# Performance work log

Hardware: AMD Instinct MI355X
Metric: run time of the kernel (lower is better)

Reference implementation:

```python
import jax, jax.numpy as jnp
import numpy as np

B, T, D, H = 256, 1024, 128, 128

def setup_inputs() -> dict:
    key = jax.random.key(0)
    k1, k2, k3, k4 = jax.random.split(key, 4)
    return {
        "x": jax.random.normal(k1, (B, T, D), dtype=jnp.float32),
        "w": jax.random.normal(k2, (D, H), dtype=jnp.float32) * 0.05,
        "state_weight": jax.random.normal(k3, (H, H), dtype=jnp.float32) * 0.05,
        "b": jax.random.normal(k4, (H,), dtype=jnp.float32) * 0.05,
    }

def reference(x, w, state_weight, b):
    # Faithful Elman RNN with return_sequences=False.
    # Original transposes input to time-major [T, B, D], initializes the
    # state from step 0 WITHOUT a recurrent term, then iterates steps 1..T-1.
    X = jnp.transpose(x, (1, 0, 2))  # [T, B, D]
    # Precompute input projections for all steps in one big GEMM (same math).
    proj = jnp.einsum("tbd,dh->tbh", X, w) + b  # [T, B, H]
    state0 = jnp.tanh(proj[0])

    def step(state, pt):
        y = jnp.tanh(pt + state @ state_weight)
        return y, None

    final_state, _ = jax.lax.scan(step, state0, proj[1:])
    return final_state  # [B, H]
```

## Files before the change

kernel.cpp:

```cpp
#include <hip/hip_runtime.h>

#define T_N 1024
#define H_N 128
#define CH   64
#define NCH (T_N / CH)
#define WPAD 136
#define PPAD 68

typedef __attribute__((ext_vector_type(8))) short bf16x8;
typedef __attribute__((ext_vector_type(4))) float f32x4;

__device__ __forceinline__ short f2bf_rne(float f) {
    union { float f; unsigned int i; } v; v.f = f;
    unsigned int r = v.i + 0x7FFFu + ((v.i >> 16) & 1u);
    return (short)(r >> 16);
}
__device__ __forceinline__ float tanh_fast(float x) {
    return 1.0f - 2.0f / (__expf(2.0f * x) + 1.0f);
}

__global__ __launch_bounds__(256, 1) void k_fused(const float* __restrict__ x,
                                                  const float* __restrict__ w,
                                                  const float* __restrict__ wst,
                                                  const float* __restrict__ bias,
                                                  float* __restrict__ out) {
    __shared__ __align__(16) short wT[H_N * WPAD];
    __shared__ __align__(16) float pT[H_N * PPAD];
    __shared__ __align__(16) short sst[2][H_N];

    const int tid  = threadIdx.x;
    const int wv   = tid >> 6;
    const int lane = tid & 63;
    const int l = lane & 15;
    const int q = lane >> 4;
    const int r = blockIdx.x;
    const float* xrow = x + (size_t)r * T_N * H_N;
    const f32x4 zero4 = (f32x4){0.f, 0.f, 0.f, 0.f};

    const float* xlane = xrow + (size_t)(wv * 16 + l) * H_N + q * 8;
    float4 xst[8];
    #pragma unroll
    for (int ks = 0; ks < 4; ++ks) {
        xst[ks * 2 + 0] = *reinterpret_cast<const float4*>(xlane + ks * 32);
        xst[ks * 2 + 1] = *reinterpret_cast<const float4*>(xlane + ks * 32 + 4);
    }

    short* wsT = reinterpret_cast<short*>(pT);
    for (int e = tid * 4; e < H_N * H_N; e += 1024) {
        int k = e >> 7, n = e & 127;
        float4 a4 = *reinterpret_cast<const float4*>(wst + e);
        wsT[(n + 0) * WPAD + k] = f2bf_rne(a4.x);
        wsT[(n + 1) * WPAD + k] = f2bf_rne(a4.y);
        wsT[(n + 2) * WPAD + k] = f2bf_rne(a4.z);
        wsT[(n + 3) * WPAD + k] = f2bf_rne(a4.w);
    }
    __syncthreads();

    bf16x8 wf[2][4];
    #pragma unroll
    for (int b = 0; b < 2; ++b)
        #pragma unroll
        for (int ks = 0; ks < 4; ++ks)
            wf[b][ks] = *reinterpret_cast<const bf16x8*>(
                &wsT[(16 * (2 * wv + b) + l) * WPAD + ks * 32 + q * 8]);
    __syncthreads();

    for (int e = tid * 4; e < H_N * H_N; e += 1024) {
        int k = e >> 7, n = e & 127;
        float4 a4 = *reinterpret_cast<const float4*>(w + e);
        wT[(n + 0) * WPAD + k] = f2bf_rne(a4.x);
        wT[(n + 1) * WPAD + k] = f2bf_rne(a4.y);
        wT[(n + 2) * WPAD + k] = f2bf_rne(a4.z);
        wT[(n + 3) * WPAD + k] = f2bf_rne(a4.w);
    }

    float bv[8];
    #pragma unroll
    for (int nt = 0; nt < 8; ++nt) bv[nt] = bias[nt * 16 + l];

    int par = 0;
    float y0 = 0.f, y1 = 0.f;
    const int row0 = (32 * wv + l) * PPAD;
    const int row1 = (32 * wv + 16 + l) * PPAD;

    #pragma unroll 1
    for (int c = 0; c < NCH; ++c) {
        bf16x8 ax[4];
        #pragma unroll
        for (int ks = 0; ks < 4; ++ks) {
            float4 u0 = xst[ks * 2 + 0];
            float4 u1 = xst[ks * 2 + 1];
            bf16x8 f;
            f[0] = f2bf_rne(u0.x); f[1] = f2bf_rne(u0.y);
            f[2] = f2bf_rne(u0.z); f[3] = f2bf_rne(u0.w);
            f[4] = f2bf_rne(u1.x); f[5] = f2bf_rne(u1.y);
            f[6] = f2bf_rne(u1.z); f[7] = f2bf_rne(u1.w);
            ax[ks] = f;
        }

        if (c + 1 < NCH) {
            const float* pn = xlane + (size_t)(c + 1) * CH * H_N;
            #pragma unroll
            for (int ks = 0; ks < 4; ++ks) {
                xst[ks * 2 + 0] = *reinterpret_cast<const float4*>(pn + ks * 32);
                xst[ks * 2 + 1] = *reinterpret_cast<const float4*>(pn + ks * 32 + 4);
            }
        }

        __syncthreads();

        #pragma unroll
        for (int nt = 0; nt < 8; ++nt) {
            f32x4 acc;
            #pragma unroll
            for (int ks = 0; ks < 4; ++ks) {
                bf16x8 bw = *reinterpret_cast<const bf16x8*>(
                    &wT[(nt * 16 + l) * WPAD + ks * 32 + q * 8]);
                acc = __builtin_amdgcn_mfma_f32_16x16x32_bf16(
                    ax[ks], bw, ks == 0 ? zero4 : acc, 0, 0, 0);
            }
            f32x4 o = (f32x4){acc[0] + bv[nt], acc[1] + bv[nt],
                              acc[2] + bv[nt], acc[3] + bv[nt]};
            *reinterpret_cast<f32x4*>(&pT[(nt * 16 + l) * PPAD + wv * 16 + q * 4]) = o;
        }

        __syncthreads();

        int tstart = 0;
        if (c == 0) {
            if (tid < 128)
                sst[0][tid] = f2bf_rne(tanh_fast(pT[tid * PPAD + 0]));
            __syncthreads();
            tstart = 1;
            par = 0;
        }

        float p0 = pT[row0 + tstart];
        float p1 = pT[row1 + tstart];

        #pragma unroll 1
        for (int t = tstart; t < CH; ++t) {
            bf16x8 a[4];
            #pragma unroll
            for (int ks = 0; ks < 4; ++ks)
                a[ks] = *reinterpret_cast<const bf16x8*>(&sst[par][ks * 32 + q * 8]);

            f32x4 acc[8];
            #pragma unroll
            for (int ks = 0; ks < 4; ++ks) {
                acc[ks]     = __builtin_amdgcn_mfma_f32_16x16x32_bf16(a[ks], wf[0][ks], zero4, 0, 0, 0);
                acc[4 + ks] = __builtin_amdgcn_mfma_f32_16x16x32_bf16(a[ks], wf[1][ks], zero4, 0, 0, 0);
            }

            int tn = (t + 1 < CH) ? t + 1 : t;
            float np0 = pT[row0 + tn];
            float np1 = pT[row1 + tn];

            float z0 = p0 + ((acc[0][0] + acc[1][0]) + (acc[2][0] + acc[3][0]));
            float z1 = p1 + ((acc[4][0] + acc[5][0]) + (acc[6][0] + acc[7][0]));
            y0 = tanh_fast(z0);
            y1 = tanh_fast(z1);
            sst[par ^ 1][32 * wv + l]      = f2bf_rne(y0);
            sst[par ^ 1][32 * wv + 16 + l] = f2bf_rne(y1);
            p0 = np0; p1 = np1;
            par ^= 1;
            __syncthreads();
        }
    }

    if (q == 0) {
        out[r * H_N + 32 * wv + l]      = y0;
        out[r * H_N + 32 * wv + 16 + l] = y1;
    }
}

extern "C" void kernel_launch(void* const* d_in, const int* in_sizes, int n_in,
                              void* d_out, int out_size, void* d_ws, size_t ws_size,
                              hipStream_t stream) {
    const float* x    = (const float*)d_in[0];
    const float* w    = (const float*)d_in[1];
    const float* wst  = (const float*)d_in[2];
    const float* bias = (const float*)d_in[3];
    float* out = (float*)d_out;

    k_fused<<<256, 256, 0, stream>>>(x, w, wst, bias, out);
}
```

Before: 444.4 us.

## Specialize waves: one runs the barrier-free recurrence, one projects the next chunk

The block shrinks to two wavefronts. Wave 0 holds the whole recurrent weight matrix in registers and runs every recurrence step alone. Because only one wave touches the state, the per-step __syncthreads and the double-buffered state disappear. Wave 1 computes the input projection for the next 64-step chunk into a double-buffered LDS tile, so that work overlaps the recurrence. In exchange, each step issues 32 serial MFMAs from a single wave instead of 8 per wave across four waves, which may lengthen the dependent chain per step.

```diff
diff --git a/kernel.cpp b/kernel.cpp
--- a/kernel.cpp
+++ b/kernel.cpp
@@ -5,7 +5,7 @@
 #define CH   64
 #define NCH (T_N / CH)
 #define WPAD 136
-#define PPAD 68
+#define TPAD 68
 
 typedef __attribute__((ext_vector_type(8))) short bf16x8;
 typedef __attribute__((ext_vector_type(4))) float f32x4;
@@ -19,14 +19,14 @@
     return 1.0f - 2.0f / (__expf(2.0f * x) + 1.0f);
 }
 
-__global__ __launch_bounds__(256, 1) void k_fused(const float* __restrict__ x,
+__global__ __launch_bounds__(128, 1) void k_fused(const float* __restrict__ x,
                                                   const float* __restrict__ w,
                                                   const float* __restrict__ wst,
                                                   const float* __restrict__ bias,
                                                   float* __restrict__ out) {
     __shared__ __align__(16) short wT[H_N * WPAD];
-    __shared__ __align__(16) float pT[H_N * PPAD];
-    __shared__ __align__(16) short sst[2][H_N];
+    __shared__ __align__(16) float pT[2][H_N * TPAD];
+    __shared__ __align__(16) short sst[H_N];
 
     const int tid  = threadIdx.x;
     const int wv   = tid >> 6;
@@ -37,35 +37,16 @@
     const float* xrow = x + (size_t)r * T_N * H_N;
     const f32x4 zero4 = (f32x4){0.f, 0.f, 0.f, 0.f};
 
-    const float* xlane = xrow + (size_t)(wv * 16 + l) * H_N + q * 8;
-    float4 xst[8];
-    #pragma unroll
-    for (int ks = 0; ks < 4; ++ks) {
-        xst[ks * 2 + 0] = *reinterpret_cast<const float4*>(xlane + ks * 32);
-        xst[ks * 2 + 1] = *reinterpret_cast<const float4*>(xlane + ks * 32 + 4);
-    }
-
-    short* wsT = reinterpret_cast<short*>(pT);
-    for (int e = tid * 4; e < H_N * H_N; e += 1024) {
+    short* wsTs = reinterpret_cast<short*>(&pT[0][0]);
+    for (int e = tid * 4; e < H_N * H_N; e += 512) {
         int k = e >> 7, n = e & 127;
         float4 a4 = *reinterpret_cast<const float4*>(wst + e);
-        wsT[(n + 0) * WPAD + k] = f2bf_rne(a4.x);
-        wsT[(n + 1) * WPAD + k] = f2bf_rne(a4.y);
-        wsT[(n + 2) * WPAD + k] = f2bf_rne(a4.z);
-        wsT[(n + 3) * WPAD + k] = f2bf_rne(a4.w);
+        wsTs[(n + 0) * WPAD + k] = f2bf_rne(a4.x);
+        wsTs[(n + 1) * WPAD + k] = f2bf_rne(a4.y);
+        wsTs[(n + 2) * WPAD + k] = f2bf_rne(a4.z);
+        wsTs[(n + 3) * WPAD + k] = f2bf_rne(a4.w);
     }
-    __syncthreads();
-
-    bf16x8 wf[2][4];
-    #pragma unroll
-    for (int b = 0; b < 2; ++b)
-        #pragma unroll
-        for (int ks = 0; ks < 4; ++ks)
-            wf[b][ks] = *reinterpret_cast<const bf16x8*>(
-                &wsT[(16 * (2 * wv + b) + l) * WPAD + ks * 32 + q * 8]);
-    __syncthreads();
-
-    for (int e = tid * 4; e < H_N * H_N; e += 1024) {
+    for (int e = tid * 4; e < H_N * H_N; e += 512) {
         int k = e >> 7, n = e & 127;
         float4 a4 = *reinterpret_cast<const float4*>(w + e);
         wT[(n + 0) * WPAD + k] = f2bf_rne(a4.x);
@@ -78,99 +59,116 @@
     #pragma unroll
     for (int nt = 0; nt < 8; ++nt) bv[nt] = bias[nt * 16 + l];
 
-    int par = 0;
+    __syncthreads();
+
+    auto do_chunk = [&](int cc, float* buf) {
+        const float* xc = xrow + (size_t)cc * CH * H_N + (size_t)l * H_N + q * 8;
+        #pragma unroll 1
+        for (int tile = 0; tile < 4; ++tile) {
+            const float* xp = xc + (size_t)tile * 16 * H_N;
+            float4 u[8];
+            #pragma unroll
+            for (int ks = 0; ks < 4; ++ks) {
+                u[2 * ks]     = *reinterpret_cast<const float4*>(xp + ks * 32);
+                u[2 * ks + 1] = *reinterpret_cast<const float4*>(xp + ks * 32 + 4);
+            }
+            bf16x8 ax[4];
+            #pragma unroll
+            for (int ks = 0; ks < 4; ++ks) {
+                float4 u0 = u[2 * ks], u1 = u[2 * ks + 1];
+                bf16x8 f;
+                f[0] = f2bf_rne(u0.x); f[1] = f2bf_rne(u0.y);
+                f[2] = f2bf_rne(u0.z); f[3] = f2bf_rne(u0.w);
+                f[4] = f2bf_rne(u1.x); f[5] = f2bf_rne(u1.y);
+                f[6] = f2bf_rne(u1.z); f[7] = f2bf_rne(u1.w);
+                ax[ks] = f;
+            }
+            #pragma unroll
+            for (int nt = 0; nt < 8; ++nt) {
+                f32x4 acc;
+                #pragma unroll
+                for (int ks = 0; ks < 4; ++ks) {
+                    bf16x8 bw = *reinterpret_cast<const bf16x8*>(
+                        &wT[(nt * 16 + l) * WPAD + ks * 32 + q * 8]);
+                    acc = __builtin_amdgcn_mfma_f32_16x16x32_bf16(
+                        ax[ks], bw, ks == 0 ? zero4 : acc, 0, 0, 0);
+                }
+                f32x4 o = (f32x4){acc[0] + bv[nt], acc[1] + bv[nt],
+                                  acc[2] + bv[nt], acc[3] + bv[nt]};
+                *reinterpret_cast<f32x4*>(
+                    &buf[(nt * 16 + l) * TPAD + tile * 16 + 4 * q]) = o;
+            }
+        }
+    };
+
+    bf16x8 wf[8][4];
+    if (wv == 0) {
+        #pragma unroll
+        for (int nt = 0; nt < 8; ++nt)
+            #pragma unroll
+            for (int ks = 0; ks < 4; ++ks)
+                wf[nt][ks] = *reinterpret_cast<const bf16x8*>(
+                    &wsTs[(16 * nt + l) * WPAD + ks * 32 + q * 8]);
+    } else {
+        do_chunk(0, &pT[1][0]);
+    }
+    __syncthreads();
+
     float y0 = 0.f, y1 = 0.f;
-    const int row0 = (32 * wv + l) * PPAD;
-    const int row1 = (32 * wv + 16 + l) * PPAD;
+    const int row0 = (32 * q + l) * TPAD;
+    const int row1 = (32 * q + 16 + l) * TPAD;
 
     #pragma unroll 1
     for (int c = 0; c < NCH; ++c) {
-        bf16x8 ax[4];
-        #pragma unroll
-        for (int ks = 0; ks < 4; ++ks) {
-            float4 u0 = xst[ks * 2 + 0];
-            float4 u1 = xst[ks * 2 + 1];
-            bf16x8 f;
-            f[0] = f2bf_rne(u0.x); f[1] = f2bf_rne(u0.y);
-            f[2] = f2bf_rne(u0.z); f[3] = f2bf_rne(u0.w);
-            f[4] = f2bf_rne(u1.x); f[5] = f2bf_rne(u1.y);
-            f[6] = f2bf_rne(u1.z); f[7] = f2bf_rne(u1.w);
-            ax[ks] = f;
+        if (wv == 0) {
+            float* pc = &pT[(c + 1) & 1][0];
+            int ts = 0;
+            if (c == 0) {
+                sst[lane]      = f2bf_rne(tanh_fast(pc[lane * TPAD]));
+                sst[64 + lane] = f2bf_rne(tanh_fast(pc[(64 + lane) * TPAD]));
+                ts = 1;
+            }
+            float p0 = pc[row0 + ts];
+            float p1 = pc[row1 + ts];
+            #pragma unroll 1
+            for (int t = ts; t < CH; ++t) {
+                bf16x8 a[4];
+                #pragma unroll
+                for (int ks = 0; ks < 4; ++ks)
+                    a[ks] = *reinterpret_cast<const bf16x8*>(&sst[ks * 32 + q * 8]);
+
+                f32x4 acc[8];
+                #pragma unroll
+                for (int nt = 0; nt < 8; ++nt) {
+                    #pragma unroll
+                    for (int ks = 0; ks < 4; ++ks)
+                        acc[nt] = __builtin_amdgcn_mfma_f32_16x16x32_bf16(
+                            a[ks], wf[nt][ks], ks == 0 ? zero4 : acc[nt], 0, 0, 0);
+                }
+
+                int tn = (t + 1 < CH) ? t + 1 : t;
+                float np0 = pc[row0 + tn];
+                float np1 = pc[row1 + tn];
+
+                float v0 = (q == 0) ? acc[0][0] : (q == 1) ? acc[2][0]
+                         : (q == 2) ? acc[4][0] : acc[6][0];
+                float v1 = (q == 0) ? acc[1][0] : (q == 1) ? acc[3][0]
+                         : (q == 2) ? acc[5][0] : acc[7][0];
+                y0 = tanh_fast(p0 + v0);
+                y1 = tanh_fast(p1 + v1);
+                sst[32 * q + l]      = f2bf_rne(y0);
+                sst[32 * q + 16 + l] = f2bf_rne(y1);
+                p0 = np0; p1 = np1;
+            }
+        } else if (c + 1 < NCH) {
+            do_chunk(c + 1, &pT[c & 1][0]);
         }
-
-        if (c + 1 < NCH) {
-            const float* pn = xlane + (size_t)(c + 1) * CH * H_N;
-            #pragma unroll
-            for (int ks = 0; ks < 4; ++ks) {
-                xst[ks * 2 + 0] = *reinterpret_cast<const float4*>(pn + ks * 32);
-                xst[ks * 2 + 1] = *reinterpret_cast<const float4*>(pn + ks * 32 + 4);
-            }
-        }
-
         __syncthreads();
-
-        #pragma unroll
-        for (int nt = 0; nt < 8; ++nt) {
-            f32x4 acc;
-            #pragma unroll
-            for (int ks = 0; ks < 4; ++ks) {
-                bf16x8 bw = *reinterpret_cast<const bf16x8*>(
-                    &wT[(nt * 16 + l) * WPAD + ks * 32 + q * 8]);
-                acc = __builtin_amdgcn_mfma_f32_16x16x32_bf16(
-                    ax[ks], bw, ks == 0 ? zero4 : acc, 0, 0, 0);
-            }
-            f32x4 o = (f32x4){acc[0] + bv[nt], acc[1] + bv[nt],
-                              acc[2] + bv[nt], acc[3] + bv[nt]};
-            *reinterpret_cast<f32x4*>(&pT[(nt * 16 + l) * PPAD + wv * 16 + q * 4]) = o;
-        }
-
-        __syncthreads();
-
-        int tstart = 0;
-        if (c == 0) {
-            if (tid < 128)
-                sst[0][tid] = f2bf_rne(tanh_fast(pT[tid * PPAD + 0]));
-            __syncthreads();
-            tstart = 1;
-            par = 0;
-        }
-
-        float p0 = pT[row0 + tstart];
-        float p1 = pT[row1 + tstart];
-
-        #pragma unroll 1
-        for (int t = tstart; t < CH; ++t) {
-            bf16x8 a[4];
-            #pragma unroll
-            for (int ks = 0; ks < 4; ++ks)
-                a[ks] = *reinterpret_cast<const bf16x8*>(&sst[par][ks * 32 + q * 8]);
-
-            f32x4 acc[8];
-            #pragma unroll
-            for (int ks = 0; ks < 4; ++ks) {
-                acc[ks]     = __builtin_amdgcn_mfma_f32_16x16x32_bf16(a[ks], wf[0][ks], zero4, 0, 0, 0);
-                acc[4 + ks] = __builtin_amdgcn_mfma_f32_16x16x32_bf16(a[ks], wf[1][ks], zero4, 0, 0, 0);
-            }
-
-            int tn = (t + 1 < CH) ? t + 1 : t;
-            float np0 = pT[row0 + tn];
-            float np1 = pT[row1 + tn];
-
-            float z0 = p0 + ((acc[0][0] + acc[1][0]) + (acc[2][0] + acc[3][0]));
-            float z1 = p1 + ((acc[4][0] + acc[5][0]) + (acc[6][0] + acc[7][0]));
-            y0 = tanh_fast(z0);
-            y1 = tanh_fast(z1);
-            sst[par ^ 1][32 * wv + l]      = f2bf_rne(y0);
-            sst[par ^ 1][32 * wv + 16 + l] = f2bf_rne(y1);
-            p0 = np0; p1 = np1;
-            par ^= 1;
-            __syncthreads();
-        }
     }
 
-    if (q == 0) {
-        out[r * H_N + 32 * wv + l]      = y0;
-        out[r * H_N + 32 * wv + 16 + l] = y1;
+    if (wv == 0) {
+        out[r * H_N + 32 * q + l]      = y0;
+        out[r * H_N + 32 * q + 16 + l] = y1;
     }
 }
 
@@ -183,5 +181,5 @@
     const float* bias = (const float*)d_in[3];
     float* out = (float*)d_out;
 
-    k_fused<<<256, 256, 0, stream>>>(x, w, wst, bias, out);
+    k_fused<<<256, 128, 0, stream>>>(x, w, wst, bias, out);
 }
```

After: 642.0 us. 1.44x slower.

## Process two batch rows per block to interleave independent recurrences

Applied to the files above, without the earlier changes.

Each block now handles two batch rows, running their recurrent MFMA chains side by side inside the same time-step loop, and the grid is halved to 128 blocks. The goal is to hide MFMA and LDS latency in the serial per-step chain by giving each wave independent work, and to share one barrier per step across two sequences. The cost is more registers and LDS (a second projection buffer and state buffer), and only 128 of the device's CUs are used where there were 256 before, so throughput can drop if per-step latency is not the bottleneck.

```diff
diff --git a/kernel.cpp b/kernel.cpp
--- a/kernel.cpp
+++ b/kernel.cpp
@@ -25,34 +25,41 @@
                                                   const float* __restrict__ bias,
                                                   float* __restrict__ out) {
     __shared__ __align__(16) short wT[H_N * WPAD];
-    __shared__ __align__(16) float pT[H_N * PPAD];
-    __shared__ __align__(16) short sst[2][H_N];
+    __shared__ __align__(16) float pTA[H_N * PPAD];
+    __shared__ __align__(16) float pTB[H_N * PPAD];
+    __shared__ __align__(16) short sstA[2][H_N];
+    __shared__ __align__(16) short sstB[2][H_N];
 
     const int tid  = threadIdx.x;
     const int wv   = tid >> 6;
     const int lane = tid & 63;
     const int l = lane & 15;
     const int q = lane >> 4;
-    const int r = blockIdx.x;
-    const float* xrow = x + (size_t)r * T_N * H_N;
+    const int r0 = blockIdx.x * 2;
+    const int r1 = r0 + 1;
+    const float* xrowA = x + (size_t)r0 * T_N * H_N;
+    const float* xrowB = x + (size_t)r1 * T_N * H_N;
     const f32x4 zero4 = (f32x4){0.f, 0.f, 0.f, 0.f};
 
-    const float* xlane = xrow + (size_t)(wv * 16 + l) * H_N + q * 8;
-    float4 xst[8];
+    const float* xlaneA = xrowA + (size_t)(wv * 16 + l) * H_N + q * 8;
+    const float* xlaneB = xrowB + (size_t)(wv * 16 + l) * H_N + q * 8;
+    float4 xstA[8], xstB[8];
     #pragma unroll
     for (int ks = 0; ks < 4; ++ks) {
-        xst[ks * 2 + 0] = *reinterpret_cast<const float4*>(xlane + ks * 32);
-        xst[ks * 2 + 1] = *reinterpret_cast<const float4*>(xlane + ks * 32 + 4);
-    }
-
-    short* wsT = reinterpret_cast<short*>(pT);
+        xstA[ks * 2 + 0] = *reinterpret_cast<const float4*>(xlaneA + ks * 32);
+        xstA[ks * 2 + 1] = *reinterpret_cast<const float4*>(xlaneA + ks * 32 + 4);
+        xstB[ks * 2 + 0] = *reinterpret_cast<const float4*>(xlaneB + ks * 32);
+        xstB[ks * 2 + 1] = *reinterpret_cast<const float4*>(xlaneB + ks * 32 + 4);
+    }
+
+    short* wsTs = reinterpret_cast<short*>(pTA);
     for (int e = tid * 4; e < H_N * H_N; e += 1024) {
         int k = e >> 7, n = e & 127;
         float4 a4 = *reinterpret_cast<const float4*>(wst + e);
-        wsT[(n + 0) * WPAD + k] = f2bf_rne(a4.x);
-        wsT[(n + 1) * WPAD + k] = f2bf_rne(a4.y);
-        wsT[(n + 2) * WPAD + k] = f2bf_rne(a4.z);
-        wsT[(n + 3) * WPAD + k] = f2bf_rne(a4.w);
+        wsTs[(n + 0) * WPAD + k] = f2bf_rne(a4.x);
+        wsTs[(n + 1) * WPAD + k] = f2bf_rne(a4.y);
+        wsTs[(n + 2) * WPAD + k] = f2bf_rne(a4.z);
+        wsTs[(n + 3) * WPAD + k] = f2bf_rne(a4.w);
     }
     __syncthreads();
 
@@ -62,7 +69,7 @@
         #pragma unroll
         for (int ks = 0; ks < 4; ++ks)
             wf[b][ks] = *reinterpret_cast<const bf16x8*>(
-                &wsT[(16 * (2 * wv + b) + l) * WPAD + ks * 32 + q * 8]);
+                &wsTs[(16 * (2 * wv + b) + l) * WPAD + ks * 32 + q * 8]);
     __syncthreads();
 
     for (int e = tid * 4; e < H_N * H_N; e += 1024) {
@@ -79,31 +86,40 @@
     for (int nt = 0; nt < 8; ++nt) bv[nt] = bias[nt * 16 + l];
 
     int par = 0;
-    float y0 = 0.f, y1 = 0.f;
+    float yA0 = 0.f, yA1 = 0.f, yB0 = 0.f, yB1 = 0.f;
     const int row0 = (32 * wv + l) * PPAD;
     const int row1 = (32 * wv + 16 + l) * PPAD;
 
     #pragma unroll 1
     for (int c = 0; c < NCH; ++c) {
-        bf16x8 ax[4];
+        bf16x8 axA[4], axB[4];
         #pragma unroll
         for (int ks = 0; ks < 4; ++ks) {
-            float4 u0 = xst[ks * 2 + 0];
-            float4 u1 = xst[ks * 2 + 1];
+            float4 u0 = xstA[ks * 2 + 0], u1 = xstA[ks * 2 + 1];
             bf16x8 f;
             f[0] = f2bf_rne(u0.x); f[1] = f2bf_rne(u0.y);
             f[2] = f2bf_rne(u0.z); f[3] = f2bf_rne(u0.w);
             f[4] = f2bf_rne(u1.x); f[5] = f2bf_rne(u1.y);
             f[6] = f2bf_rne(u1.z); f[7] = f2bf_rne(u1.w);
-            ax[ks] = f;
+            axA[ks] = f;
+            float4 v0 = xstB[ks * 2 + 0], v1 = xstB[ks * 2 + 1];
+            bf16x8 g;
+            g[0] = f2bf_rne(v0.x); g[1] = f2bf_rne(v0.y);
+            g[2] = f2bf_rne(v0.z); g[3] = f2bf_rne(v0.w);
+            g[4] = f2bf_rne(v1.x); g[5] = f2bf_rne(v1.y);
+            g[6] = f2bf_rne(v1.z); g[7] = f2bf_rne(v1.w);
+            axB[ks] = g;
         }
 
         if (c + 1 < NCH) {
-            const float* pn = xlane + (size_t)(c + 1) * CH * H_N;
-            #pragma unroll
-            for (int ks = 0; ks < 4; ++ks) {
-                xst[ks * 2 + 0] = *reinterpret_cast<const float4*>(pn + ks * 32);
-                xst[ks * 2 + 1] = *reinterpret_cast<const float4*>(pn + ks * 32 + 4);
+            const float* pnA = xlaneA + (size_t)(c + 1) * CH * H_N;
+            const float* pnB = xlaneB + (size_t)(c + 1) * CH * H_N;
+            #pragma unroll
+            for (int ks = 0; ks < 4; ++ks) {
+                xstA[ks * 2 + 0] = *reinterpret_cast<const float4*>(pnA + ks * 32);
+                xstA[ks * 2 + 1] = *reinterpret_cast<const float4*>(pnA + ks * 32 + 4);
+                xstB[ks * 2 + 0] = *reinterpret_cast<const float4*>(pnB + ks * 32);
+                xstB[ks * 2 + 1] = *reinterpret_cast<const float4*>(pnB + ks * 32 + 4);
             }
         }
 
@@ -111,17 +127,22 @@
 
         #pragma unroll
         for (int nt = 0; nt < 8; ++nt) {
-            f32x4 acc;
+            f32x4 aA, aB;
             #pragma unroll
             for (int ks = 0; ks < 4; ++ks) {
                 bf16x8 bw = *reinterpret_cast<const bf16x8*>(
                     &wT[(nt * 16 + l) * WPAD + ks * 32 + q * 8]);
-                acc = __builtin_amdgcn_mfma_f32_16x16x32_bf16(
-                    ax[ks], bw, ks == 0 ? zero4 : acc, 0, 0, 0);
-            }
-            f32x4 o = (f32x4){acc[0] + bv[nt], acc[1] + bv[nt],
-                              acc[2] + bv[nt], acc[3] + bv[nt]};
-            *reinterpret_cast<f32x4*>(&pT[(nt * 16 + l) * PPAD + wv * 16 + q * 4]) = o;
+                aA = __builtin_amdgcn_mfma_f32_16x16x32_bf16(
+                    axA[ks], bw, ks == 0 ? zero4 : aA, 0, 0, 0);
+                aB = __builtin_amdgcn_mfma_f32_16x16x32_bf16(
+                    axB[ks], bw, ks == 0 ? zero4 : aB, 0, 0, 0);
+            }
+            f32x4 oA = (f32x4){aA[0] + bv[nt], aA[1] + bv[nt],
+                               aA[2] + bv[nt], aA[3] + bv[nt]};
+            f32x4 oB = (f32x4){aB[0] + bv[nt], aB[1] + bv[nt],
+                               aB[2] + bv[nt], aB[3] + bv[nt]};
+            *reinterpret_cast<f32x4*>(&pTA[(nt * 16 + l) * PPAD + wv * 16 + q * 4]) = oA;
+            *reinterpret_cast<f32x4*>(&pTB[(nt * 16 + l) * PPAD + wv * 16 + q * 4]) = oB;
         }
 
         __syncthreads();
@@ -129,48 +150,75 @@
         int tstart = 0;
         if (c == 0) {
             if (tid < 128)
-                sst[0][tid] = f2bf_rne(tanh_fast(pT[tid * PPAD + 0]));
+                sstA[0][tid] = f2bf_rne(tanh_fast(pTA[tid * PPAD + 0]));
+            else {
+                int u = tid - 128;
+                sstB[0][u] = f2bf_rne(tanh_fast(pTB[u * PPAD + 0]));
+            }
             __syncthreads();
             tstart = 1;
             par = 0;
         }
 
-        float p0 = pT[row0 + tstart];
-        float p1 = pT[row1 + tstart];
+        float pA0 = pTA[row0 + tstart];
+        float pA1 = pTA[row1 + tstart];
+        float pB0 = pTB[row0 + tstart];
+        float pB1 = pTB[row1 + tstart];
 
         #pragma unroll 1
         for (int t = tstart; t < CH; ++t) {
-            bf16x8 a[4];
+            bf16x8 aA[4], aB[4];
             #pragma unroll
             for (int ks = 0; ks < 4; ++ks)
-                a[ks] = *reinterpret_cast<const bf16x8*>(&sst[par][ks * 32 + q * 8]);
-
-            f32x4 acc[8];
-            #pragma unroll
-            for (int ks = 0; ks < 4; ++ks) {
-                acc[ks]     = __builtin_amdgcn_mfma_f32_16x16x32_bf16(a[ks], wf[0][ks], zero4, 0, 0, 0);
-                acc[4 + ks] = __builtin_amdgcn_mfma_f32_16x16x32_bf16(a[ks], wf[1][ks], zero4, 0, 0, 0);
+                aA[ks] = *reinterpret_cast<const bf16x8*>(&sstA[par][ks * 32 + q * 8]);
+            #pragma unroll
+            for (int ks = 0; ks < 4; ++ks)
+                aB[ks] = *reinterpret_cast<const bf16x8*>(&sstB[par][ks * 32 + q * 8]);
+
+            f32x4 accA[8];
+            #pragma unroll
+            for (int ks = 0; ks < 4; ++ks) {
+                accA[ks]     = __builtin_amdgcn_mfma_f32_16x16x32_bf16(aA[ks], wf[0][ks], zero4, 0, 0, 0);
+                accA[4 + ks] = __builtin_amdgcn_mfma_f32_16x16x32_bf16(aA[ks], wf[1][ks], zero4, 0, 0, 0);
+            }
+            f32x4 accB[8];
+            #pragma unroll
+            for (int ks = 0; ks < 4; ++ks) {
+                accB[ks]     = __builtin_amdgcn_mfma_f32_16x16x32_bf16(aB[ks], wf[0][ks], zero4, 0, 0, 0);
+                accB[4 + ks] = __builtin_amdgcn_mfma_f32_16x16x32_bf16(aB[ks], wf[1][ks], zero4, 0, 0, 0);
             }
 
             int tn = (t + 1 < CH) ? t + 1 : t;
-            float np0 = pT[row0 + tn];
-            float np1 = pT[row1 + tn];
-
-            float z0 = p0 + ((acc[0][0] + acc[1][0]) + (acc[2][0] + acc[3][0]));
-            float z1 = p1 + ((acc[4][0] + acc[5][0]) + (acc[6][0] + acc[7][0]));
-            y0 = tanh_fast(z0);
-            y1 = tanh_fast(z1);
-            sst[par ^ 1][32 * wv + l]      = f2bf_rne(y0);
-            sst[par ^ 1][32 * wv + 16 + l] = f2bf_rne(y1);
-            p0 = np0; p1 = np1;
+            float npA0 = pTA[row0 + tn];
+            float npA1 = pTA[row1 + tn];
+            float npB0 = pTB[row0 + tn];
+            float npB1 = pTB[row1 + tn];
+
+            float zA0 = pA0 + ((accA[0][0] + accA[1][0]) + (accA[2][0] + accA[3][0]));
+            float zA1 = pA1 + ((accA[4][0] + accA[5][0]) + (accA[6][0] + accA[7][0]));
+            yA0 = tanh_fast(zA0);
+            yA1 = tanh_fast(zA1);
+            sstA[par ^ 1][32 * wv + l]      = f2bf_rne(yA0);
+            sstA[par ^ 1][32 * wv + 16 + l] = f2bf_rne(yA1);
+
+            float zB0 = pB0 + ((accB[0][0] + accB[1][0]) + (accB[2][0] + accB[3][0]));
+            float zB1 = pB1 + ((accB[4][0] + accB[5][0]) + (accB[6][0] + accB[7][0]));
+            yB0 = tanh_fast(zB0);
+            yB1 = tanh_fast(zB1);
+            sstB[par ^ 1][32 * wv + l]      = f2bf_rne(yB0);
+            sstB[par ^ 1][32 * wv + 16 + l] = f2bf_rne(yB1);
+
+            pA0 = npA0; pA1 = npA1; pB0 = npB0; pB1 = npB1;
             par ^= 1;
             __syncthreads();
         }
     }
 
     if (q == 0) {
-        out[r * H_N + 32 * wv + l]      = y0;
-        out[r * H_N + 32 * wv + 16 + l] = y1;
+        out[r0 * H_N + 32 * wv + l]      = yA0;
+        out[r0 * H_N + 32 * wv + 16 + l] = yA1;
+        out[r1 * H_N + 32 * wv + l]      = yB0;
+        out[r1 * H_N + 32 * wv + 16 + l] = yB1;
     }
 }
 
@@ -183,5 +231,5 @@
     const float* bias = (const float*)d_in[3];
     float* out = (float*)d_out;
 
-    k_fused<<<256, 256, 0, stream>>>(x, w, wst, bias, out);
-}
+    k_fused<<<128, 256, 0, stream>>>(x, w, wst, bias, out);
+}
```

Result: slower. 698.6 us (+57.2%).

## Split recurrent work across eight waves per block instead of four

Applied to the files above, without the earlier changes.

Doubles the block to 512 threads so each wave owns one 16-column slice of the recurrent matmul instead of two. Per-step MFMA count and tanh work per wave are halved, which shortens the serial per-timestep critical path. Input projection work is split by time tile and column half across wave pairs. The cost is a barrier synchronising twice as many waves every timestep, plus duplicate x loads per wave pair.

```diff
diff --git a/kernel.cpp b/kernel.cpp
--- a/kernel.cpp
+++ b/kernel.cpp
@@ -19,7 +19,7 @@
     return 1.0f - 2.0f / (__expf(2.0f * x) + 1.0f);
 }
 
-__global__ __launch_bounds__(256, 1) void k_fused(const float* __restrict__ x,
+__global__ __launch_bounds__(512, 1) void k_fused(const float* __restrict__ x,
                                                   const float* __restrict__ w,
                                                   const float* __restrict__ wst,
                                                   const float* __restrict__ bias,
@@ -33,11 +33,13 @@
     const int lane = tid & 63;
     const int l = lane & 15;
     const int q = lane >> 4;
+    const int tt = wv >> 1;
+    const int h  = wv & 1;
     const int r = blockIdx.x;
     const float* xrow = x + (size_t)r * T_N * H_N;
     const f32x4 zero4 = (f32x4){0.f, 0.f, 0.f, 0.f};
 
-    const float* xlane = xrow + (size_t)(wv * 16 + l) * H_N + q * 8;
+    const float* xlane = xrow + (size_t)(tt * 16 + l) * H_N + q * 8;
     float4 xst[8];
     #pragma unroll
     for (int ks = 0; ks < 4; ++ks) {
@@ -45,27 +47,25 @@
         xst[ks * 2 + 1] = *reinterpret_cast<const float4*>(xlane + ks * 32 + 4);
     }
 
-    short* wsT = reinterpret_cast<short*>(pT);
-    for (int e = tid * 4; e < H_N * H_N; e += 1024) {
+    short* wsTs = reinterpret_cast<short*>(pT);
+    for (int e = tid * 4; e < H_N * H_N; e += 2048) {
         int k = e >> 7, n = e & 127;
         float4 a4 = *reinterpret_cast<const float4*>(wst + e);
-        wsT[(n + 0) * WPAD + k] = f2bf_rne(a4.x);
-        wsT[(n + 1) * WPAD + k] = f2bf_rne(a4.y);
-        wsT[(n + 2) * WPAD + k] = f2bf_rne(a4.z);
-        wsT[(n + 3) * WPAD + k] = f2bf_rne(a4.w);
+        wsTs[(n + 0) * WPAD + k] = f2bf_rne(a4.x);
+        wsTs[(n + 1) * WPAD + k] = f2bf_rne(a4.y);
+        wsTs[(n + 2) * WPAD + k] = f2bf_rne(a4.z);
+        wsTs[(n + 3) * WPAD + k] = f2bf_rne(a4.w);
     }
     __syncthreads();
 
-    bf16x8 wf[2][4];
+    bf16x8 wf[4];
     #pragma unroll
-    for (int b = 0; b < 2; ++b)
-        #pragma unroll
-        for (int ks = 0; ks < 4; ++ks)
-            wf[b][ks] = *reinterpret_cast<const bf16x8*>(
-                &wsT[(16 * (2 * wv + b) + l) * WPAD + ks * 32 + q * 8]);
+    for (int ks = 0; ks < 4; ++ks)
+        wf[ks] = *reinterpret_cast<const bf16x8*>(
+            &wsTs[(16 * wv + l) * WPAD + ks * 32 + q * 8]);
     __syncthreads();
 
-    for (int e = tid * 4; e < H_N * H_N; e += 1024) {
+    for (int e = tid * 4; e < H_N * H_N; e += 2048) {
         int k = e >> 7, n = e & 127;
         float4 a4 = *reinterpret_cast<const float4*>(w + e);
         wT[(n + 0) * WPAD + k] = f2bf_rne(a4.x);
@@ -74,14 +74,13 @@
         wT[(n + 3) * WPAD + k] = f2bf_rne(a4.w);
     }
 
-    float bv[8];
+    float bv[4];
     #pragma unroll
-    for (int nt = 0; nt < 8; ++nt) bv[nt] = bias[nt * 16 + l];
+    for (int j = 0; j < 4; ++j) bv[j] = bias[(4 * h + j) * 16 + l];
 
     int par = 0;
-    float y0 = 0.f, y1 = 0.f;
-    const int row0 = (32 * wv + l) * PPAD;
-    const int row1 = (32 * wv + 16 + l) * PPAD;
+    float y = 0.f;
+    const int rowp = (16 * wv + l) * PPAD;
 
     #pragma unroll 1
     for (int c = 0; c < NCH; ++c) {
@@ -110,7 +109,8 @@
         __syncthreads();
 
         #pragma unroll
-        for (int nt = 0; nt < 8; ++nt) {
+        for (int j = 0; j < 4; ++j) {
+            const int nt = 4 * h + j;
             f32x4 acc;
             #pragma unroll
             for (int ks = 0; ks < 4; ++ks) {
@@ -119,9 +119,9 @@
                 acc = __builtin_amdgcn_mfma_f32_16x16x32_bf16(
                     ax[ks], bw, ks == 0 ? zero4 : acc, 0, 0, 0);
             }
-            f32x4 o = (f32x4){acc[0] + bv[nt], acc[1] + bv[nt],
-                              acc[2] + bv[nt], acc[3] + bv[nt]};
-            *reinterpret_cast<f32x4*>(&pT[(nt * 16 + l) * PPAD + wv * 16 + q * 4]) = o;
+            f32x4 o = (f32x4){acc[0] + bv[j], acc[1] + bv[j],
+                              acc[2] + bv[j], acc[3] + bv[j]};
+            *reinterpret_cast<f32x4*>(&pT[(nt * 16 + l) * PPAD + tt * 16 + q * 4]) = o;
         }
 
         __syncthreads();
@@ -135,8 +135,7 @@
             par = 0;
         }
 
-        float p0 = pT[row0 + tstart];
-        float p1 = pT[row1 + tstart];
+        float p = pT[rowp + tstart];
 
         #pragma unroll 1
         for (int t = tstart; t < CH; ++t) {
@@ -145,33 +144,27 @@
             for (int ks = 0; ks < 4; ++ks)
                 a[ks] = *reinterpret_cast<const bf16x8*>(&sst[par][ks * 32 + q * 8]);
 
-            f32x4 acc[8];
+            f32x4 acc[4];
             #pragma unroll
-            for (int ks = 0; ks < 4; ++ks) {
-                acc[ks]     = __builtin_amdgcn_mfma_f32_16x16x32_bf16(a[ks], wf[0][ks], zero4, 0, 0, 0);
-                acc[4 + ks] = __builtin_amdgcn_mfma_f32_16x16x32_bf16(a[ks], wf[1][ks], zero4, 0, 0, 0);
-            }
+            for (int ks = 0; ks < 4; ++ks)
+                acc[ks] = __builtin_amdgcn_mfma_f32_16x16x32_bf16(
+                    a[ks], wf[ks], zero4, 0, 0, 0);
 
             int tn = (t + 1 < CH) ? t + 1 : t;
-            float np0 = pT[row0 + tn];
-            float np1 = pT[row1 + tn];
+            float np = pT[rowp + tn];
 
-            float z0 = p0 + ((acc[0][0] + acc[1][0]) + (acc[2][0] + acc[3][0]));
-            float z1 = p1 + ((acc[4][0] + acc[5][0]) + (acc[6][0] + acc[7][0]));
-            y0 = tanh_fast(z0);
-            y1 = tanh_fast(z1);
-            sst[par ^ 1][32 * wv + l]      = f2bf_rne(y0);
-            sst[par ^ 1][32 * wv + 16 + l] = f2bf_rne(y1);
-            p0 = np0; p1 = np1;
+            float z = p + ((acc[0][0] + acc[1][0]) + (acc[2][0] + acc[3][0]));
+            y = tanh_fast(z);
+            if (q == 0)
+                sst[par ^ 1][16 * wv + l] = f2bf_rne(y);
+            p = np;
             par ^= 1;
             __syncthreads();
         }
     }
 
-    if (q == 0) {
-        out[r * H_N + 32 * wv + l]      = y0;
-        out[r * H_N + 32 * wv + 16 + l] = y1;
-    }
+    if (q == 0)
+        out[r * H_N + 16 * wv + l] = y;
 }
 
 extern "C" void kernel_launch(void* const* d_in, const int* in_sizes, int n_in,
@@ -183,5 +176,5 @@
     const float* bias = (const float*)d_in[3];
     float* out = (float*)d_out;
 
-    k_fused<<<256, 256, 0, stream>>>(x, w, wst, bias, out);
+    k_fused<<<256, 512, 0, stream>>>(x, w, wst, bias, out);
 }
```

Result: no change. 448.3 us (+0.9%).
